# Kernel tuning notes

Hardware: AMD Instinct MI355X
Metric: run time of the kernel (lower is better)

## Reference

```python
import jax, jax.numpy as jnp
import numpy as np

EPS = 1e-5  # nn.BatchNorm2d default eps


def _cbs(x, w, g, b, m, v):
    # Conv(k=1, bias=False) + BatchNorm2d(inference) + SiLU
    y = jnp.einsum('bchw,oc->bohw', x, w)
    s = (g * jax.lax.rsqrt(v + EPS))[None, :, None, None]
    y = (y - m[None, :, None, None]) * s + b[None, :, None, None]
    return y * jax.nn.sigmoid(y)


def setup_inputs():
    key = jax.random.key(0)
    B, D, H, W = 1, 256, 80, 80
    C = D // 2
    ks = jax.random.split(key, 20)
    r = lambda i, shape, sc=1.0: jax.random.normal(ks[i], shape, dtype=jnp.float32) * sc
    oC, oD = jnp.ones((C,), jnp.float32), jnp.ones((D,), jnp.float32)
    zC, zD = jnp.zeros((C,), jnp.float32), jnp.zeros((D,), jnp.float32)
    return {
        'x': r(0, (B, D, H, W)),
        'w1': r(1, (C, D), 0.05), 'g1': oC, 'b1': zC, 'm1': zC, 'v1': oC,
        'w2': r(2, (D, C), 0.05), 'g2': oD, 'b2': zD, 'm2': zD, 'v2': oD,
        'w3': r(3, (D, C), 0.05), 'g3': oD, 'b3': zD, 'm3': zD, 'v3': oD,
        'wq': r(4, (C, C), 0.05), 'bq': r(5, (C,), 0.01),
        'wk': r(6, (C, C), 0.05), 'bk': r(7, (C,), 0.01),
        'wv': r(8, (C, C), 0.05), 'bv': r(9, (C,), 0.01),
        'wp': r(10, (C, C), 0.05), 'bp': r(11, (C,), 0.01),
        'rel_h': r(12, (1, C, H, 1)), 'rel_w': r(13, (1, C, 1, W)),
        'ef_h': r(14, (1, C, H, 1)), 'ef_w': r(15, (1, C, 1, W)),
    }


def reference(x, w1, g1, b1, m1, v1, w2, g2, b2, m2, v2, w3, g3, b3, m3, v3,
              wq, bq, wk, bk, wv, bv, wp, bp, rel_h, rel_w, ef_h, ef_w):
    x1 = _cbs(x, w1, g1, b1, m1, v1)            # [B, C, H, W]
    B, C, H, W = x1.shape
    HW = H * W
    proj = lambda w, b: (jnp.einsum('bchw,oc->bohw', x1, w)
                         + b[None, :, None, None]).reshape(B, C, HW)
    q = proj(wq, bq)
    k = proj(wk, bk)
    v = proj(wv, bv)
    p = proj(wp, bp)
    # content-content + content-position attention branch
    cp = (rel_h + rel_w).reshape(C, HW)          # [C, HW]
    cc = jnp.einsum('bci,bcj->bij', q, k)        # [B, HW, HW]
    cpos = jnp.einsum('ci,bcj->bij', cp, q)      # [B, HW, HW]
    attn = jax.nn.softmax(cc + cpos, axis=-1)
    # out1[b,c,i] = sum_j v[b,c,j] * attn[b,i,j]  (bmm(v, attn^T))
    out1 = jnp.einsum('bcj,bij->bci', v, attn).reshape(B, C, H, W)
    # extra positional branch (valid because B == 1)
    ef = (ef_h + ef_w).reshape(B, C, HW)         # [1, C, HW]
    ce = jnp.einsum('bci,bcj->bij', p, ef)       # [B, HW, HW]
    eng = jax.nn.softmax(ce, axis=-1)
    out2 = jnp.einsum('bcj,bij->bci', ef, eng).reshape(B, C, H, W)
    return x + _cbs(out1, w2, g2, b2, m2, v2) + _cbs(out2, w3, g3, b3, m3, v3)
```

## Files before the change

### kernel.cpp

```cpp
#include <hip/hip_runtime.h>


typedef unsigned short u16;
typedef __attribute__((ext_vector_type(8))) short bf16x8;
typedef __attribute__((ext_vector_type(4))) float f32x4;
typedef __attribute__((ext_vector_type(4))) unsigned int u32x4;

#define HW 6400
#define BN_EPS 1e-5f

__device__ __forceinline__ u16 f2b(float f) {
  unsigned u = __float_as_uint(f);
  u += 0x7fffu + ((u >> 16) & 1u);
  return (u16)(u >> 16);
}
__device__ __forceinline__ unsigned pack2(float a, float b) {
  return (unsigned)f2b(a) | ((unsigned)f2b(b) << 16);
}
__device__ __forceinline__ f32x4 MFMA(bf16x8 a, bf16x8 b, f32x4 c) {
  return __builtin_amdgcn_mfma_f32_16x16x32_bf16(a, b, c, 0, 0, 0);
}
__device__ __forceinline__ float silu_f(float y) {
  return y / (1.0f + __expf(-y));
}
__device__ __forceinline__ bf16x8 pack8(f32x4 lo, f32x4 hi, float sc) {
  union { bf16x8 v; uint4 u; } r;
  r.u.x = pack2(lo[0] * sc, lo[1] * sc);
  r.u.y = pack2(lo[2] * sc, lo[3] * sc);
  r.u.z = pack2(hi[0] * sc, hi[1] * sc);
  r.u.w = pack2(hi[2] * sc, hi[3] * sc);
  return r.v;
}
__device__ __forceinline__ void gload_lds16(const u16* src, u16* dst) {
  __builtin_amdgcn_global_load_lds(
      (const __attribute__((address_space(1))) void*)src,
      (__attribute__((address_space(3))) void*)dst, 16, 0, 0);
}

__global__ void prep_all(
    const float* __restrict__ rel_h, const float* __restrict__ rel_w,
    const float* __restrict__ ef_h, const float* __restrict__ ef_w,
    const float* __restrict__ w1, const float* __restrict__ g1, const float* __restrict__ b1,
    const float* __restrict__ m1, const float* __restrict__ v1,
    const float* __restrict__ w2, const float* __restrict__ g2, const float* __restrict__ b2,
    const float* __restrict__ m2, const float* __restrict__ v2,
    const float* __restrict__ w3, const float* __restrict__ g3, const float* __restrict__ b3,
    const float* __restrict__ m3, const float* __restrict__ v3,
    const float* __restrict__ wq, const float* __restrict__ bq,
    const float* __restrict__ wk, const float* __restrict__ bk,
    const float* __restrict__ wv, const float* __restrict__ bv,
    const float* __restrict__ wp, const float* __restrict__ bp,
    u16* __restrict__ LT,
    u16* __restrict__ w1b, float* __restrict__ b1e,
    u16* __restrict__ Wcat, float* __restrict__ bcat,
    u16* __restrict__ w2b, float* __restrict__ b2e,
    u16* __restrict__ w3b, float* __restrict__ b3e,
    u16* __restrict__ efhT, u16* __restrict__ efwT,
    u16* __restrict__ efhB, u16* __restrict__ efwB,
    u16* __restrict__ expA, u16* __restrict__ expB,
    float* __restrict__ lbuf)
{
  const int b = blockIdx.x;
  const int t = threadIdx.x;
  if (b < 80) {
    const int h = b;
    const int c0 = (t & 63) * 2;
    const float rh0 = rel_h[c0 * 80 + h], rh1 = rel_h[(c0 + 1) * 80 + h];
    for (int wcol = (t >> 6); wcol < 80; wcol += 4) {
      const int i = h * 80 + wcol;
      float rw0 = rel_w[c0 * 80 + wcol], rw1 = rel_w[(c0 + 1) * 80 + wcol];
      *(unsigned*)&LT[(size_t)i * 256 + 128 + c0] = pack2(rh0 + rw0, rh1 + rw1);
    }
  } else if (b < 144) {
    const int tid = (b - 80) * 256 + t;
    const int stride = 64 * 256;
    for (int idx = tid; idx < 128 * 256; idx += stride) {
      int o = idx >> 8;
      float s = g1[o] * rsqrtf(v1[o] + BN_EPS);
      w1b[idx] = f2b(w1[idx] * s);
    }
    for (int idx = tid; idx < 128; idx += stride) {
      float s = g1[idx] * rsqrtf(v1[idx] + BN_EPS);
      b1e[idx] = b1[idx] - m1[idx] * s;
    }
    for (int idx = tid; idx < 4 * 128 * 128; idx += stride) {
      int which = idx >> 14, r = idx & 16383;
      const float* src = which == 0 ? wq : which == 1 ? wk : which == 2 ? wv : wp;
      Wcat[idx] = f2b(src[r]);
    }
    for (int idx = tid; idx < 512; idx += stride) {
      int which = idx >> 7, r = idx & 127;
      const float* src = which == 0 ? bq : which == 1 ? bk : which == 2 ? bv : bp;
      bcat[idx] = src[r];
    }
    for (int idx = tid; idx < 256 * 128; idx += stride) {
      int o = idx >> 7;
      float s2 = g2[o] * rsqrtf(v2[o] + BN_EPS);
      w2b[idx] = f2b(w2[idx] * s2);
      float s3 = g3[o] * rsqrtf(v3[o] + BN_EPS);
      w3b[idx] = f2b(w3[idx] * s3);
    }
    for (int idx = tid; idx < 256; idx += stride) {
      float s2 = g2[idx] * rsqrtf(v2[idx] + BN_EPS);
      b2e[idx] = b2[idx] - m2[idx] * s2;
      float s3 = g3[idx] * rsqrtf(v3[idx] + BN_EPS);
      b3e[idx] = b3[idx] - m3[idx] * s3;
    }
    for (int idx = tid; idx < 80 * 128; idx += stride) {
      int hj = idx >> 7, c = idx & 127;
      efhT[idx] = f2b(ef_h[c * 80 + hj]);
      efwT[idx] = f2b(ef_w[c * 80 + hj]);
    }
    for (int idx = tid; idx < 128 * 96; idx += stride) {
      int c = idx / 96, hj = idx % 96;
      efhB[idx] = hj < 80 ? f2b(ef_h[c * 80 + hj]) : (u16)0;
      efwB[idx] = hj < 80 ? f2b(ef_w[c * 80 + hj]) : (u16)0;
    }
  } else {
    const int tid = (b - 144) * 256 + t;
    const int stride = 32 * 256;
    for (int idx = tid; idx < HW / 4; idx += stride)
      ((f32x4*)lbuf)[idx] = (f32x4){0.f, 0.f, 0.f, 0.f};
    for (int idx = tid; idx < HW * 96 / 8; idx += stride) {
      ((u32x4*)expA)[idx] = (u32x4){0, 0, 0, 0};
      ((u32x4*)expB)[idx] = (u32x4){0, 0, 0, 0};
    }
  }
}

__global__ __launch_bounds__(64) void front_k(
    const float* __restrict__ x,
    const u16* __restrict__ w1b, const float* __restrict__ b1e,
    const u16* __restrict__ Wcat, const float* __restrict__ bcat,
    u16* __restrict__ LT, u16* __restrict__ RT, u16* __restrict__ Vv,
    u16* __restrict__ pT)
{
  __shared__ __align__(16) u16 tr[16][136];
  const int t = threadIdx.x, lane = t & 63, jl = lane & 15, q = lane >> 4;
  const int i0 = blockIdx.x * 16;

  bf16x8 afr[8];
#pragma unroll
  for (int ks = 0; ks < 8; ++ks) {
    union { bf16x8 v; u16 e[8]; } fa;
#pragma unroll
    for (int e = 0; e < 8; ++e)
      fa.e[e] = f2b(x[(size_t)(ks * 32 + q * 8 + e) * HW + i0 + jl]);
    afr[ks] = fa.v;
  }
  f32x4 acc[8];
#pragma unroll
  for (int nf = 0; nf < 8; ++nf) acc[nf] = (f32x4){0.f, 0.f, 0.f, 0.f};
#pragma unroll
  for (int ks = 0; ks < 8; ++ks)
#pragma unroll
    for (int nf = 0; nf < 8; ++nf) {
      bf16x8 b = *(const bf16x8*)(w1b + (size_t)(nf * 16 + jl) * 256 + ks * 32 + q * 8);
      acc[nf] = MFMA(afr[ks], b, acc[nf]);
    }
#pragma unroll
  for (int nf = 0; nf < 8; ++nf) {
    const int c = nf * 16 + jl;
    const float bias = b1e[c];
#pragma unroll
    for (int r = 0; r < 4; ++r)
      tr[q * 4 + r][c] = f2b(silu_f(acc[nf][r] + bias));
  }
  __syncthreads();
  bf16x8 xa[4];
#pragma unroll
  for (int ks = 0; ks < 4; ++ks)
    xa[ks] = *(const bf16x8*)&tr[jl][ks * 32 + q * 8];

#pragma unroll
  for (int nc = 0; nc < 4; ++nc) {
    f32x4 a2[8];
#pragma unroll
    for (int nf = 0; nf < 8; ++nf) a2[nf] = (f32x4){0.f, 0.f, 0.f, 0.f};
#pragma unroll
    for (int ks = 0; ks < 4; ++ks)
#pragma unroll
      for (int nf = 0; nf < 8; ++nf) {
        bf16x8 b = *(const bf16x8*)(Wcat + (size_t)(nc * 128 + nf * 16 + jl) * 128 + ks * 32 + q * 8);
        a2[nf] = MFMA(xa[ks], b, a2[nf]);
      }
    if (nc == 2) {
#pragma unroll
      for (int nf = 0; nf < 8; ++nf) {
        const int c = nf * 16 + jl;
        const float bias = bcat[256 + c];
        uint2 pk;
        pk.x = pack2(a2[nf][0] + bias, a2[nf][1] + bias);
        pk.y = pack2(a2[nf][2] + bias, a2[nf][3] + bias);
        *(uint2*)(Vv + (size_t)c * HW + i0 + q * 4) = pk;
      }
    } else {
      __syncthreads();
#pragma unroll
      for (int nf = 0; nf < 8; ++nf) {
        const int c = nf * 16 + jl;
        const float bias = bcat[nc * 128 + c];
#pragma unroll
        for (int r = 0; r < 4; ++r)
          tr[q * 4 + r][c] = f2b(a2[nf][r] + bias);
      }
      __syncthreads();
#pragma unroll
      for (int r = 0; r < 16; ++r) {
        unsigned val = *(const unsigned*)&tr[r][lane * 2];
        const size_t row = (size_t)(i0 + r);
        if (nc == 0) {
          *(unsigned*)(LT + row * 256 + lane * 2) = val;
          *(unsigned*)(RT + row * 256 + 128 + lane * 2) = val;
        } else if (nc == 1) {
          *(unsigned*)(RT + row * 256 + lane * 2) = val;
        } else {
          *(unsigned*)(pT + row * 128 + lane * 2) = val;
        }
      }
    }
  }
}

__global__ __launch_bounds__(256) void sep2a(
    const u16* __restrict__ pT,
    const u16* __restrict__ efhT,
    const u16* __restrict__ efwT,
    u16* __restrict__ expA, u16* __restrict__ expB,
    float* __restrict__ sA, float* __restrict__ sB)
{
  const int t = threadIdx.x, lane = t & 63, w = t >> 6, jl = lane & 15, q = lane >> 4;
  const int i0w = blockIdx.x * 128 + w * 32;

  bf16x8 pfr[2][4];
#pragma unroll
  for (int mt = 0; mt < 2; ++mt)
#pragma unroll
    for (int l = 0; l < 4; ++l)
      pfr[mt][l] = *(const bf16x8*)(pT + (size_t)(i0w + mt * 16 + jl) * 128 + l * 32 + q * 8);

  f32x4 sa[5][2], sb[5][2];
#pragma unroll
  for (int nf = 0; nf < 5; ++nf)
#pragma unroll
    for (int mt = 0; mt < 2; ++mt) {
      sa[nf][mt] = (f32x4){0.f, 0.f, 0.f, 0.f};
      sb[nf][mt] = (f32x4){0.f, 0.f, 0.f, 0.f};
    }
#pragma unroll
  for (int nf = 0; nf < 5; ++nf) {
    const int row = nf * 16 + jl;
#pragma unroll
    for (int l = 0; l < 4; ++l) {
      bf16x8 eh = *(const bf16x8*)(efhT + (size_t)row * 128 + l * 32 + q * 8);
      bf16x8 ew = *(const bf16x8*)(efwT + (size_t)row * 128 + l * 32 + q * 8);
      sa[nf][0] = MFMA(eh, pfr[0][l], sa[nf][0]);
      sa[nf][1] = MFMA(eh, pfr[1][l], sa[nf][1]);
      sb[nf][0] = MFMA(ew, pfr[0][l], sb[nf][0]);
      sb[nf][1] = MFMA(ew, pfr[1][l], sb[nf][1]);
    }
  }
#pragma unroll
  for (int mt = 0; mt < 2; ++mt) {
    const int i = i0w + mt * 16 + jl;
    float ra = 0.f, rb = 0.f;
#pragma unroll
    for (int nf = 0; nf < 5; ++nf) {
      float ea[4], eb[4];
#pragma unroll
      for (int r = 0; r < 4; ++r) {
        ea[r] = __expf(sa[nf][mt][r]); ra += ea[r];
        eb[r] = __expf(sb[nf][mt][r]); rb += eb[r];
      }
      uint2 pa, pb;
      pa.x = pack2(ea[0], ea[1]); pa.y = pack2(ea[2], ea[3]);
      pb.x = pack2(eb[0], eb[1]); pb.y = pack2(eb[2], eb[3]);
      *(uint2*)(expA + (size_t)i * 96 + nf * 16 + q * 4) = pa;
      *(uint2*)(expB + (size_t)i * 96 + nf * 16 + q * 4) = pb;
    }
    ra += __shfl_xor(ra, 16); ra += __shfl_xor(ra, 32);
    rb += __shfl_xor(rb, 16); rb += __shfl_xor(rb, 32);
    if (lane < 16) { sA[i] = ra; sB[i] = rb; }
  }
}

__global__ __launch_bounds__(256) void sep2b(
    const u16* __restrict__ expA, const u16* __restrict__ expB,
    const float* __restrict__ sA, const float* __restrict__ sB,
    const u16* __restrict__ efhB, const u16* __restrict__ efwB,
    u16* __restrict__ Ob2)
{
  const int t = threadIdx.x, lane = t & 63, w = t >> 6, jl = lane & 15, q = lane >> 4;
  const int i0w = blockIdx.x * 128 + w * 32;

#pragma unroll
  for (int mt = 0; mt < 2; ++mt) {
    bf16x8 fa[3], fb[3];
#pragma unroll
    for (int l = 0; l < 3; ++l) {
      fa[l] = *(const bf16x8*)(expA + (size_t)(i0w + mt * 16 + jl) * 96 + l * 32 + q * 8);
      fb[l] = *(const bf16x8*)(expB + (size_t)(i0w + mt * 16 + jl) * 96 + l * 32 + q * 8);
    }
    f32x4 oU[8], oW[8];
#pragma unroll
    for (int nf = 0; nf < 8; ++nf) {
      oU[nf] = (f32x4){0.f, 0.f, 0.f, 0.f};
      oW[nf] = (f32x4){0.f, 0.f, 0.f, 0.f};
    }
#pragma unroll
    for (int l = 0; l < 3; ++l)
#pragma unroll
      for (int nf = 0; nf < 8; ++nf) {
        bf16x8 bh = *(const bf16x8*)(efhB + (size_t)(nf * 16 + jl) * 96 + l * 32 + q * 8);
        bf16x8 bw = *(const bf16x8*)(efwB + (size_t)(nf * 16 + jl) * 96 + l * 32 + q * 8);
        oU[nf] = MFMA(fa[l], bh, oU[nf]);
        oW[nf] = MFMA(fb[l], bw, oW[nf]);
      }
    const int ib = i0w + mt * 16 + q * 4;
    float ia[4], iw[4];
#pragma unroll
    for (int r = 0; r < 4; ++r) {
      ia[r] = 1.0f / sA[ib + r];
      iw[r] = 1.0f / sB[ib + r];
    }
#pragma unroll
    for (int nf = 0; nf < 8; ++nf)
#pragma unroll
      for (int r = 0; r < 4; ++r)
        Ob2[(size_t)(ib + r) * 128 + nf * 16 + jl] =
            f2b(oU[nf][r] * ia[r] + oW[nf][r] * iw[r]);
  }
}

__global__ __launch_bounds__(512, 2) void fused_attn(
    const u16* __restrict__ LT,
    const u16* __restrict__ RT,
    const u16* __restrict__ Vv,
    float* __restrict__ Opart,
    float* __restrict__ lv)
{
  __shared__ __align__(1024) u16 Rs[2][128 * 128];
  __shared__ __align__(1024) u16 Ts[2][64 * 128];
  const int t = threadIdx.x, lane = t & 63, w = t >> 6, jl = lane & 15, q = lane >> 4;
  const int it = blockIdx.x / 10, jp = blockIdx.x % 10;
  const int wi = w & 1, wj = w >> 1;
  const int i0w = it * 128 + wi * 64;
  u16* Tw = Ts[wi];

  bf16x8 afr[4][8];
#pragma unroll
  for (int mt = 0; mt < 4; ++mt)
#pragma unroll
    for (int l = 0; l < 8; ++l)
      afr[mt][l] = *(const bf16x8*)(LT + (size_t)(i0w + mt * 16 + jl) * 256 + l * 32 + q * 8);

  f32x4 o[4][2];
#pragma unroll
  for (int mt = 0; mt < 4; ++mt)
#pragma unroll
    for (int cf = 0; cf < 2; ++cf) o[mt][cf] = (f32x4){0.f, 0.f, 0.f, 0.f};
  float lacc[4] = {0.f, 0.f, 0.f, 0.f};

  auto stage = [&](int jj) {
#pragma unroll
    for (int k = 0; k < 8; ++k) {
      const int b = k >> 2, cl = k & 3;
      const int cc = w * 4 + cl;
      const int jr = cc * 4 + (lane >> 4);
      const int cp = lane & 15;
      const int ch = (cp & ~7) | ((cp ^ jr) & 7);
      gload_lds16(RT + (size_t)(jj + jr) * 256 + b * 128 + ch * 8,
                  Rs[b] + (cc << 9));
    }
  };

  stage(jp * 640);

  for (int stp = 0; stp < 5; ++stp) {
    const int jj = jp * 640 + stp * 128;

    f32x4 s[2][4];
#pragma unroll
    for (int nf = 0; nf < 2; ++nf)
#pragma unroll
      for (int mt = 0; mt < 4; ++mt) s[nf][mt] = (f32x4){0.f, 0.f, 0.f, 0.f};

    __syncthreads();

#pragma unroll
    for (int h = 0; h < 2; ++h)
#pragma unroll
      for (int nf = 0; nf < 2; ++nf) {
        const int row = wj * 32 + nf * 16 + jl;
#pragma unroll
        for (int l = 0; l < 4; ++l) {
          const int ch = (l * 4 + q) ^ (jl & 7);
          bf16x8 b = *(const bf16x8*)(Rs[h] + row * 128 + ch * 8);
          s[nf][0] = MFMA(b, afr[0][h * 4 + l], s[nf][0]);
          s[nf][1] = MFMA(b, afr[1][h * 4 + l], s[nf][1]);
          s[nf][2] = MFMA(b, afr[2][h * 4 + l], s[nf][2]);
          s[nf][3] = MFMA(b, afr[3][h * 4 + l], s[nf][3]);
        }
      }
    __syncthreads();
    if (stp < 4) stage(jj + 128);

#pragma unroll
    for (int nf = 0; nf < 2; ++nf)
#pragma unroll
      for (int mt = 0; mt < 4; ++mt)
#pragma unroll
        for (int r = 0; r < 4; ++r) {
          float p = __expf(s[nf][mt][r]);
          s[nf][mt][r] = p;
          lacc[mt] += p;
        }

#pragma unroll
    for (int mt = 0; mt < 4; ++mt)
#pragma unroll
      for (int nf = 0; nf < 2; ++nf) {
        const int row = mt * 16 + jl;
        const int cs = (wj * 8 + nf * 4 + q) ^ ((jl & 7) << 2);
        uint2 pk;
        pk.x = pack2(s[nf][mt][0], s[nf][mt][1]);
        pk.y = pack2(s[nf][mt][2], s[nf][mt][3]);
        *(uint2*)(Tw + row * 128 + cs * 4) = pk;
      }
    __syncthreads();

#pragma unroll
    for (int ks2 = 0; ks2 < 4; ++ks2) {
      bf16x8 bv0 = *(const bf16x8*)(Vv + (size_t)(wj * 32 + jl) * HW + jj + ks2 * 32 + q * 8);
      bf16x8 bv1 = *(const bf16x8*)(Vv + (size_t)(wj * 32 + 16 + jl) * HW + jj + ks2 * 32 + q * 8);
      const int cb = (ks2 * 8 + q * 2) ^ ((jl & 7) << 2);
#pragma unroll
      for (int mt = 0; mt < 4; ++mt) {
        bf16x8 pa = *(const bf16x8*)(Tw + (mt * 16 + jl) * 128 + cb * 4);
        o[mt][0] = MFMA(pa, bv0, o[mt][0]);
        o[mt][1] = MFMA(pa, bv1, o[mt][1]);
      }
    }
  }

#pragma unroll
  for (int mt = 0; mt < 4; ++mt) {
    float rsum = lacc[mt];
    rsum += __shfl_xor(rsum, 16);
    rsum += __shfl_xor(rsum, 32);
    if (lane < 16)
      atomicAdd(&lv[i0w + mt * 16 + jl], rsum);
  }
  float* Op = Opart + (size_t)jp * HW * 128;
#pragma unroll
  for (int mt = 0; mt < 4; ++mt) {
    const int ib = i0w + mt * 16 + q * 4;
#pragma unroll
    for (int cf = 0; cf < 2; ++cf) {
      const int c = wj * 32 + cf * 16 + jl;
#pragma unroll
      for (int r = 0; r < 4; ++r)
        Op[(size_t)(ib + r) * 128 + c] = o[mt][cf][r];
    }
  }
}

__global__ __launch_bounds__(256) void red_k(
    const float* __restrict__ Opart,
    const float* __restrict__ lv,
    u16* __restrict__ Ob1)
{
  const int idx = blockIdx.x * 256 + threadIdx.x;
  const int i = idx >> 4;
  const int c0 = (idx & 15) * 8;
  f32x4 a = {0.f, 0.f, 0.f, 0.f}, b = {0.f, 0.f, 0.f, 0.f};
#pragma unroll
  for (int p = 0; p < 10; ++p) {
    const float* src = Opart + ((size_t)p * HW + i) * 128 + c0;
    a += *(const f32x4*)src;
    b += *(const f32x4*)(src + 4);
  }
  const float inv = 1.0f / lv[i];
  *(bf16x8*)(Ob1 + (size_t)i * 128 + c0) = pack8(a, b, inv);
}

__global__ __launch_bounds__(256) void final_k(
    const u16* __restrict__ Ob1,
    const u16* __restrict__ Ob2,
    const u16* __restrict__ w2b, const float* __restrict__ b2e,
    const u16* __restrict__ w3b, const float* __restrict__ b3e,
    const float* __restrict__ x, float* __restrict__ outp)
{
  const int t = threadIdx.x, w = t >> 6, lane = t & 63, jl = lane & 15, q = lane >> 4;
  const int i0 = blockIdx.x * 64 + w * 16;
  const int nc = blockIdx.y;
  const int row = i0 + jl;

  f32x4 a1[8], a2[8];
#pragma unroll
  for (int nf = 0; nf < 8; ++nf) {
    a1[nf] = (f32x4){0.f, 0.f, 0.f, 0.f};
    a2[nf] = (f32x4){0.f, 0.f, 0.f, 0.f};
  }
#pragma unroll
  for (int ks = 0; ks < 4; ++ks) {
    bf16x8 fa1 = *(const bf16x8*)(Ob1 + (size_t)row * 128 + ks * 32 + q * 8);
    bf16x8 fa2 = *(const bf16x8*)(Ob2 + (size_t)row * 128 + ks * 32 + q * 8);
#pragma unroll
    for (int nf = 0; nf < 8; ++nf) {
      bf16x8 b2f = *(const bf16x8*)(w2b + (size_t)(nc * 128 + nf * 16 + jl) * 128 + ks * 32 + q * 8);
      bf16x8 b3f = *(const bf16x8*)(w3b + (size_t)(nc * 128 + nf * 16 + jl) * 128 + ks * 32 + q * 8);
      a1[nf] = MFMA(fa1, b2f, a1[nf]);
      a2[nf] = MFMA(fa2, b3f, a2[nf]);
    }
  }
#pragma unroll
  for (int nf = 0; nf < 8; ++nf) {
    const int d = nc * 128 + nf * 16 + jl;
    const float bb2 = b2e[d], bb3 = b3e[d];
    const size_t base = (size_t)d * HW + i0 + q * 4;
    f32x4 xv = *(const f32x4*)(x + base);
    f32x4 rv;
#pragma unroll
    for (int r = 0; r < 4; ++r)
      rv[r] = xv[r] + silu_f(a1[nf][r] + bb2) + silu_f(a2[nf][r] + bb3);
    *(f32x4*)(outp + base) = rv;
  }
}

extern "C" void kernel_launch(void* const* d_in, const int* in_sizes, int n_in,
                              void* d_out, int out_size, void* d_ws, size_t ws_size,
                              hipStream_t stream)
{
  (void)in_sizes; (void)n_in; (void)out_size; (void)ws_size;
  const float* x   = (const float*)d_in[0];
  const float* w1  = (const float*)d_in[1];
  const float* g1  = (const float*)d_in[2];
  const float* b1  = (const float*)d_in[3];
  const float* m1  = (const float*)d_in[4];
  const float* v1  = (const float*)d_in[5];
  const float* w2  = (const float*)d_in[6];
  const float* g2  = (const float*)d_in[7];
  const float* b2  = (const float*)d_in[8];
  const float* m2  = (const float*)d_in[9];
  const float* v2  = (const float*)d_in[10];
  const float* w3  = (const float*)d_in[11];
  const float* g3  = (const float*)d_in[12];
  const float* b3  = (const float*)d_in[13];
  const float* m3  = (const float*)d_in[14];
  const float* v3  = (const float*)d_in[15];
  const float* wq  = (const float*)d_in[16];
  const float* bq  = (const float*)d_in[17];
  const float* wk  = (const float*)d_in[18];
  const float* bk  = (const float*)d_in[19];
  const float* wv  = (const float*)d_in[20];
  const float* bv  = (const float*)d_in[21];
  const float* wp  = (const float*)d_in[22];
  const float* bp  = (const float*)d_in[23];
  const float* rel_h = (const float*)d_in[24];
  const float* rel_w = (const float*)d_in[25];
  const float* ef_h  = (const float*)d_in[26];
  const float* ef_w  = (const float*)d_in[27];
  float* outp = (float*)d_out;

  char* ws = (char*)d_ws;
  size_t off = 0;
  auto alloc = [&](size_t bytes) -> void* {
    void* p = ws + off;
    off += (bytes + 511) & ~(size_t)511;
    return p;
  };
  u16* LT    = (u16*)alloc((size_t)HW * 256 * 2);
  u16* RT    = (u16*)alloc((size_t)HW * 256 * 2);
  u16* pT    = (u16*)alloc((size_t)HW * 128 * 2);
  u16* Vv    = (u16*)alloc((size_t)HW * 128 * 2);
  float* Opart = (float*)alloc((size_t)10 * HW * 128 * 4);
  u16* Ob1   = (u16*)alloc((size_t)HW * 128 * 2);
  u16* Ob2   = (u16*)alloc((size_t)HW * 128 * 2);
  float* lbuf  = (float*)alloc((size_t)HW * 4);
  u16* w1b   = (u16*)alloc(128 * 256 * 2);
  float* b1e = (float*)alloc(128 * 4);
  u16* Wcat  = (u16*)alloc(512 * 128 * 2);
  float* bcat = (float*)alloc(512 * 4);
  u16* w2b   = (u16*)alloc(256 * 128 * 2);
  float* b2e = (float*)alloc(256 * 4);
  u16* w3b   = (u16*)alloc(256 * 128 * 2);
  float* b3e = (float*)alloc(256 * 4);
  u16* efhT  = (u16*)alloc(80 * 128 * 2);
  u16* efwT  = (u16*)alloc(80 * 128 * 2);
  u16* efhB  = (u16*)alloc(128 * 96 * 2);
  u16* efwB  = (u16*)alloc(128 * 96 * 2);
  u16* expA  = (u16*)alloc((size_t)HW * 96 * 2);
  u16* expB  = (u16*)alloc((size_t)HW * 96 * 2);
  float* sA  = (float*)alloc(HW * 4);
  float* sB  = (float*)alloc(HW * 4);

  prep_all<<<176, 256, 0, stream>>>(rel_h, rel_w, ef_h, ef_w,
                                    w1, g1, b1, m1, v1, w2, g2, b2, m2, v2,
                                    w3, g3, b3, m3, v3, wq, bq, wk, bk, wv, bv, wp, bp,
                                    LT, w1b, b1e, Wcat, bcat, w2b, b2e, w3b, b3e,
                                    efhT, efwT, efhB, efwB, expA, expB, lbuf);
  front_k<<<400, 64, 0, stream>>>(x, w1b, b1e, Wcat, bcat, LT, RT, Vv, pT);
  sep2a<<<50, 256, 0, stream>>>(pT, efhT, efwT, expA, expB, sA, sB);
  sep2b<<<50, 256, 0, stream>>>(expA, expB, sA, sB, efhB, efwB, Ob2);
  fused_attn<<<500, 512, 0, stream>>>(LT, RT, Vv, Opart, lbuf);
  red_k<<<400, 256, 0, stream>>>(Opart, lbuf, Ob1);
  final_k<<<dim3(100, 2), 256, 0, stream>>>(Ob1, Ob2, w2b, b2e, w3b, b3e, x, outp);
}
```

Measured before the change: 249.9 us.

## Fold sep2a into attention launch and merge reduction and sep2b into final kernel

The sep2a work now runs as 25 extra blocks inside the fused_attn launch. sep2a_body uses 512 threads with 256 rows per block, so the 256-thread kernel's wave layout changes. The split-K reduction, sep2b and the final conv are merged into one final2 kernel, with Opart re-laid out per row so the partials can be summed in registers. front_k now stages x through shared memory with vectorised loads instead of strided scalar loads. This removes three launches and the Ob1/Ob2 round-trips, but the final kernel repeats sep2b work for each of the two nc halves.

```diff
diff --git a/kernel.cpp b/kernel.cpp
--- a/kernel.cpp
+++ b/kernel.cpp
@@ -135,18 +135,27 @@
     u16* __restrict__ LT, u16* __restrict__ RT, u16* __restrict__ Vv,
     u16* __restrict__ pT)
 {
+  __shared__ __align__(16) float xs[16][260];
   __shared__ __align__(16) u16 tr[16][136];
   const int t = threadIdx.x, lane = t & 63, jl = lane & 15, q = lane >> 4;
   const int i0 = blockIdx.x * 16;
 
+#pragma unroll
+  for (int p = 0; p < 16; ++p) {
+    const int ch = p * 16 + (lane >> 2);
+    const int ii = (lane & 3) * 4;
+    f32x4 v = *(const f32x4*)(x + (size_t)ch * HW + i0 + ii);
+    xs[ii][ch] = v[0]; xs[ii + 1][ch] = v[1];
+    xs[ii + 2][ch] = v[2]; xs[ii + 3][ch] = v[3];
+  }
+  __syncthreads();
+
   bf16x8 afr[8];
 #pragma unroll
   for (int ks = 0; ks < 8; ++ks) {
-    union { bf16x8 v; u16 e[8]; } fa;
-#pragma unroll
-    for (int e = 0; e < 8; ++e)
-      fa.e[e] = f2b(x[(size_t)(ks * 32 + q * 8 + e) * HW + i0 + jl]);
-    afr[ks] = fa.v;
+    f32x4 va = *(const f32x4*)&xs[jl][ks * 32 + q * 8];
+    f32x4 vb = *(const f32x4*)&xs[jl][ks * 32 + q * 8 + 4];
+    afr[ks] = pack8(va, vb, 1.0f);
   }
   f32x4 acc[8];
 #pragma unroll
@@ -222,15 +231,15 @@
   }
 }
 
-__global__ __launch_bounds__(256) void sep2a(
-    const u16* __restrict__ pT,
-    const u16* __restrict__ efhT,
+__device__ __forceinline__ void sep2a_body(
+    int b2,
+    const u16* __restrict__ pT, const u16* __restrict__ efhT,
     const u16* __restrict__ efwT,
     u16* __restrict__ expA, u16* __restrict__ expB,
     float* __restrict__ sA, float* __restrict__ sB)
 {
   const int t = threadIdx.x, lane = t & 63, w = t >> 6, jl = lane & 15, q = lane >> 4;
-  const int i0w = blockIdx.x * 128 + w * 32;
+  const int i0w = b2 * 256 + w * 32;
 
   bf16x8 pfr[2][4];
 #pragma unroll
@@ -284,65 +293,26 @@
   }
 }
 
-__global__ __launch_bounds__(256) void sep2b(
-    const u16* __restrict__ expA, const u16* __restrict__ expB,
-    const float* __restrict__ sA, const float* __restrict__ sB,
-    const u16* __restrict__ efhB, const u16* __restrict__ efwB,
-    u16* __restrict__ Ob2)
-{
-  const int t = threadIdx.x, lane = t & 63, w = t >> 6, jl = lane & 15, q = lane >> 4;
-  const int i0w = blockIdx.x * 128 + w * 32;
-
-#pragma unroll
-  for (int mt = 0; mt < 2; ++mt) {
-    bf16x8 fa[3], fb[3];
-#pragma unroll
-    for (int l = 0; l < 3; ++l) {
-      fa[l] = *(const bf16x8*)(expA + (size_t)(i0w + mt * 16 + jl) * 96 + l * 32 + q * 8);
-      fb[l] = *(const bf16x8*)(expB + (size_t)(i0w + mt * 16 + jl) * 96 + l * 32 + q * 8);
-    }
-    f32x4 oU[8], oW[8];
-#pragma unroll
-    for (int nf = 0; nf < 8; ++nf) {
-      oU[nf] = (f32x4){0.f, 0.f, 0.f, 0.f};
-      oW[nf] = (f32x4){0.f, 0.f, 0.f, 0.f};
-    }
-#pragma unroll
-    for (int l = 0; l < 3; ++l)
-#pragma unroll
-      for (int nf = 0; nf < 8; ++nf) {
-        bf16x8 bh = *(const bf16x8*)(efhB + (size_t)(nf * 16 + jl) * 96 + l * 32 + q * 8);
-        bf16x8 bw = *(const bf16x8*)(efwB + (size_t)(nf * 16 + jl) * 96 + l * 32 + q * 8);
-        oU[nf] = MFMA(fa[l], bh, oU[nf]);
-        oW[nf] = MFMA(fb[l], bw, oW[nf]);
-      }
-    const int ib = i0w + mt * 16 + q * 4;
-    float ia[4], iw[4];
-#pragma unroll
-    for (int r = 0; r < 4; ++r) {
-      ia[r] = 1.0f / sA[ib + r];
-      iw[r] = 1.0f / sB[ib + r];
-    }
-#pragma unroll
-    for (int nf = 0; nf < 8; ++nf)
-#pragma unroll
-      for (int r = 0; r < 4; ++r)
-        Ob2[(size_t)(ib + r) * 128 + nf * 16 + jl] =
-            f2b(oU[nf][r] * ia[r] + oW[nf][r] * iw[r]);
-  }
-}
-
 __global__ __launch_bounds__(512, 2) void fused_attn(
     const u16* __restrict__ LT,
     const u16* __restrict__ RT,
     const u16* __restrict__ Vv,
     float* __restrict__ Opart,
-    float* __restrict__ lv)
+    float* __restrict__ lv,
+    const u16* __restrict__ pT, const u16* __restrict__ efhT,
+    const u16* __restrict__ efwT,
+    u16* __restrict__ expA, u16* __restrict__ expB,
+    float* __restrict__ sA, float* __restrict__ sB)
 {
   __shared__ __align__(1024) u16 Rs[2][128 * 128];
   __shared__ __align__(1024) u16 Ts[2][64 * 128];
+  const int bid = blockIdx.x;
+  if (bid >= 500) {
+    sep2a_body(bid - 500, pT, efhT, efwT, expA, expB, sA, sB);
+    return;
+  }
   const int t = threadIdx.x, lane = t & 63, w = t >> 6, jl = lane & 15, q = lane >> 4;
-  const int it = blockIdx.x / 10, jp = blockIdx.x % 10;
+  const int it = bid / 10, jp = bid % 10;
   const int wi = w & 1, wj = w >> 1;
   const int i0w = it * 128 + wi * 64;
   u16* Tw = Ts[wi];
@@ -451,7 +421,6 @@
     if (lane < 16)
       atomicAdd(&lv[i0w + mt * 16 + jl], rsum);
   }
-  float* Op = Opart + (size_t)jp * HW * 128;
 #pragma unroll
   for (int mt = 0; mt < 4; ++mt) {
     const int ib = i0w + mt * 16 + q * 4;
@@ -460,42 +429,67 @@
       const int c = wj * 32 + cf * 16 + jl;
 #pragma unroll
       for (int r = 0; r < 4; ++r)
-        Op[(size_t)(ib + r) * 128 + c] = o[mt][cf][r];
-    }
-  }
-}
-
-__global__ __launch_bounds__(256) void red_k(
+        Opart[((size_t)(ib + r) * 10 + jp) * 128 + c] = o[mt][cf][r];
+    }
+  }
+}
+
+__global__ __launch_bounds__(256) void final2(
+    const u16* __restrict__ expA, const u16* __restrict__ expB,
+    const float* __restrict__ sA, const float* __restrict__ sB,
+    const u16* __restrict__ efhB, const u16* __restrict__ efwB,
     const float* __restrict__ Opart,
     const float* __restrict__ lv,
-    u16* __restrict__ Ob1)
-{
-  const int idx = blockIdx.x * 256 + threadIdx.x;
-  const int i = idx >> 4;
-  const int c0 = (idx & 15) * 8;
-  f32x4 a = {0.f, 0.f, 0.f, 0.f}, b = {0.f, 0.f, 0.f, 0.f};
-#pragma unroll
-  for (int p = 0; p < 10; ++p) {
-    const float* src = Opart + ((size_t)p * HW + i) * 128 + c0;
-    a += *(const f32x4*)src;
-    b += *(const f32x4*)(src + 4);
-  }
-  const float inv = 1.0f / lv[i];
-  *(bf16x8*)(Ob1 + (size_t)i * 128 + c0) = pack8(a, b, inv);
-}
-
-__global__ __launch_bounds__(256) void final_k(
-    const u16* __restrict__ Ob1,
-    const u16* __restrict__ Ob2,
     const u16* __restrict__ w2b, const float* __restrict__ b2e,
     const u16* __restrict__ w3b, const float* __restrict__ b3e,
     const float* __restrict__ x, float* __restrict__ outp)
 {
-  const int t = threadIdx.x, w = t >> 6, lane = t & 63, jl = lane & 15, q = lane >> 4;
-  const int i0 = blockIdx.x * 64 + w * 16;
+  __shared__ __align__(16) u16 T2[64][136];
+  const int t = threadIdx.x, lane = t & 63, w = t >> 6, jl = lane & 15, q = lane >> 4;
+  const int i0 = blockIdx.x * 64;
   const int nc = blockIdx.y;
-  const int row = i0 + jl;
-
+  const int rowA = i0 + w * 16 + jl;
+
+  {
+    bf16x8 fa[3], fb[3];
+#pragma unroll
+    for (int l = 0; l < 3; ++l) {
+      fa[l] = *(const bf16x8*)(expA + (size_t)rowA * 96 + l * 32 + q * 8);
+      fb[l] = *(const bf16x8*)(expB + (size_t)rowA * 96 + l * 32 + q * 8);
+    }
+    f32x4 oU[8], oW[8];
+#pragma unroll
+    for (int nf = 0; nf < 8; ++nf) {
+      oU[nf] = (f32x4){0.f, 0.f, 0.f, 0.f};
+      oW[nf] = (f32x4){0.f, 0.f, 0.f, 0.f};
+    }
+#pragma unroll
+    for (int l = 0; l < 3; ++l)
+#pragma unroll
+      for (int nf = 0; nf < 8; ++nf) {
+        bf16x8 bh = *(const bf16x8*)(efhB + (size_t)(nf * 16 + jl) * 96 + l * 32 + q * 8);
+        bf16x8 bw = *(const bf16x8*)(efwB + (size_t)(nf * 16 + jl) * 96 + l * 32 + q * 8);
+        oU[nf] = MFMA(fa[l], bh, oU[nf]);
+        oW[nf] = MFMA(fb[l], bw, oW[nf]);
+      }
+    const int ib = i0 + w * 16 + q * 4;
+    float ia[4], iw[4];
+#pragma unroll
+    for (int r = 0; r < 4; ++r) {
+      ia[r] = 1.0f / sA[ib + r];
+      iw[r] = 1.0f / sB[ib + r];
+    }
+#pragma unroll
+    for (int nf = 0; nf < 8; ++nf)
+#pragma unroll
+      for (int r = 0; r < 4; ++r)
+        T2[w * 16 + q * 4 + r][nf * 16 + jl] =
+            f2b(oU[nf][r] * ia[r] + oW[nf][r] * iw[r]);
+  }
+  __syncthreads();
+
+  const float inv1 = 1.0f / lv[rowA];
+  const float* OrBase = Opart + (size_t)rowA * 10 * 128;
   f32x4 a1[8], a2[8];
 #pragma unroll
   for (int nf = 0; nf < 8; ++nf) {
@@ -504,8 +498,16 @@
   }
 #pragma unroll
   for (int ks = 0; ks < 4; ++ks) {
-    bf16x8 fa1 = *(const bf16x8*)(Ob1 + (size_t)row * 128 + ks * 32 + q * 8);
-    bf16x8 fa2 = *(const bf16x8*)(Ob2 + (size_t)row * 128 + ks * 32 + q * 8);
+    f32x4 s1a = (f32x4){0.f, 0.f, 0.f, 0.f};
+    f32x4 s1b = (f32x4){0.f, 0.f, 0.f, 0.f};
+#pragma unroll
+    for (int p = 0; p < 10; ++p) {
+      const float* Or = OrBase + p * 128;
+      s1a += *(const f32x4*)(Or + ks * 32 + q * 8);
+      s1b += *(const f32x4*)(Or + ks * 32 + q * 8 + 4);
+    }
+    bf16x8 fa1 = pack8(s1a, s1b, inv1);
+    bf16x8 fa2 = *(const bf16x8*)&T2[w * 16 + jl][ks * 32 + q * 8];
 #pragma unroll
     for (int nf = 0; nf < 8; ++nf) {
       bf16x8 b2f = *(const bf16x8*)(w2b + (size_t)(nc * 128 + nf * 16 + jl) * 128 + ks * 32 + q * 8);
@@ -518,7 +520,7 @@
   for (int nf = 0; nf < 8; ++nf) {
     const int d = nc * 128 + nf * 16 + jl;
     const float bb2 = b2e[d], bb3 = b3e[d];
-    const size_t base = (size_t)d * HW + i0 + q * 4;
+    const size_t base = (size_t)d * HW + i0 + w * 16 + q * 4;
     f32x4 xv = *(const f32x4*)(x + base);
     f32x4 rv;
 #pragma unroll
@@ -574,9 +576,7 @@
   u16* RT    = (u16*)alloc((size_t)HW * 256 * 2);
   u16* pT    = (u16*)alloc((size_t)HW * 128 * 2);
   u16* Vv    = (u16*)alloc((size_t)HW * 128 * 2);
-  float* Opart = (float*)alloc((size_t)10 * HW * 128 * 4);
-  u16* Ob1   = (u16*)alloc((size_t)HW * 128 * 2);
-  u16* Ob2   = (u16*)alloc((size_t)HW * 128 * 2);
+  float* Opart = (float*)alloc((size_t)HW * 10 * 128 * 4);
   float* lbuf  = (float*)alloc((size_t)HW * 4);
   u16* w1b   = (u16*)alloc(128 * 256 * 2);
   float* b1e = (float*)alloc(128 * 4);
@@ -601,9 +601,9 @@
                                     LT, w1b, b1e, Wcat, bcat, w2b, b2e, w3b, b3e,
                                     efhT, efwT, efhB, efwB, expA, expB, lbuf);
   front_k<<<400, 64, 0, stream>>>(x, w1b, b1e, Wcat, bcat, LT, RT, Vv, pT);
-  sep2a<<<50, 256, 0, stream>>>(pT, efhT, efwT, expA, expB, sA, sB);
-  sep2b<<<50, 256, 0, stream>>>(expA, expB, sA, sB, efhB, efwB, Ob2);
-  fused_attn<<<500, 512, 0, stream>>>(LT, RT, Vv, Opart, lbuf);
-  red_k<<<400, 256, 0, stream>>>(Opart, lbuf, Ob1);
-  final_k<<<dim3(100, 2), 256, 0, stream>>>(Ob1, Ob2, w2b, b2e, w3b, b3e, x, outp);
-}
+  fused_attn<<<525, 512, 0, stream>>>(LT, RT, Vv, Opart, lbuf,
+                                      pT, efhT, efwT, expA, expB, sA, sB);
+  final2<<<dim3(100, 2), 256, 0, stream>>>(expA, expB, sA, sB, efhB, efwB,
+                                           Opart, lbuf, w2b, b2e, w3b, b3e,
+                                           x, outp);
+}
```

After: 250.9 us. Within noise of the previous version (+0.4%).
